# Optimization experiments

Measured on AMD Instinct MI355X. Metric: run time of the kernel, lower is better.

## Reference

```python
import jax, jax.numpy as jnp
import numpy as np

B, T, H = 32, 4096, 512
K = 11  # conv kernel size, 'same' padding


def setup_inputs() -> dict:
    key = jax.random.key(0)
    k1, k2, k3, k4, k5 = jax.random.split(key, 5)
    eh = jax.random.normal(k1, (B, T, H), dtype=jnp.float32)
    dhx = jax.random.normal(k2, (B, H), dtype=jnp.float32)
    ax = jax.random.uniform(k3, (B, T), dtype=jnp.float32)
    conv_w = jax.random.normal(k4, (1, 1, K), dtype=jnp.float32) * 0.1
    conv_b = jax.random.normal(k5, (1,), dtype=jnp.float32) * 0.1
    return {"eh": eh, "dhx": dhx, "ax": ax, "conv_w": conv_w, "conv_b": conv_b}


def reference(eh, dhx, ax, conv_w, conv_b):
    # content score: (B,T,H) . (B,H) -> (B,T)
    pax = jnp.einsum('bth,bh->bt', eh, dhx)
    # location bias: 1D 'same' conv on previous attention vector
    pad = (K - 1) // 2
    loc = jax.lax.conv_general_dilated(
        ax[:, None, :], conv_w,
        window_strides=(1,), padding=[(pad, pad)],
        dimension_numbers=('NCH', 'OIH', 'NCH'))[:, 0, :] + conv_b
    pax = pax + loc
    # softmax over time axis (legacy F.softmax on 2D -> dim=1)
    a = jax.nn.softmax(pax, axis=1)
    # summary: weighted sum over time -> (B,H)
    sx = jnp.einsum('bth,bt->bh', eh, a)
    return (sx, a)
```

## Files before the change

kernel.cpp:

```cpp
#include <hip/hip_runtime.h>
#include <cfloat>

#define BB 32
#define TT 4096
#define HH 512
#define KSZ 11
#define PAD 5
#define TCHUNK 128
#define NCHUNK (TT / TCHUNK)
#define NWAVES 4
#define ROWS_PER_WAVE (TCHUNK / NWAVES)

__global__ __launch_bounds__(256) void attn_pass1(
    const float* __restrict__ eh, const float* __restrict__ dhx,
    const float* __restrict__ ax, const float* __restrict__ conv_w,
    const float* __restrict__ conv_b,
    float* __restrict__ pax_ws, float* __restrict__ part_m,
    float* __restrict__ part_l, float* __restrict__ part_acc)
{
    const int bid  = blockIdx.x;
    const int b    = bid / NCHUNK;
    const int c    = bid % NCHUNK;
    const int tid  = threadIdx.x;
    const int wave = tid >> 6;
    const int lane = tid & 63;

    __shared__ float s_loc[TCHUNK];
    __shared__ float red_m[NWAVES], red_l[NWAVES];
    __shared__ float red_acc[NWAVES][HH];

    if (tid < TCHUNK) {
        const int t = c * TCHUNK + tid;
        float locv = conv_b[0];
        #pragma unroll
        for (int k = 0; k < KSZ; ++k) {
            const int ts = t + k - PAD;
            const float v = (ts >= 0 && ts < TT) ? ax[b * TT + ts] : 0.0f;
            locv = fmaf(v, conv_w[k], locv);
        }
        s_loc[tid] = locv;
    }

    const float4* dp = (const float4*)(dhx + (size_t)b * HH + lane * 8);
    const float4 d0 = dp[0];
    const float4 d1 = dp[1];

    __syncthreads();

    float m = -FLT_MAX, l = 0.0f;
    float acc[8];
    #pragma unroll
    for (int j = 0; j < 8; ++j) acc[j] = 0.0f;

    const int t0 = c * TCHUNK + wave * ROWS_PER_WAVE;
    for (int r = 0; r < ROWS_PER_WAVE; ++r) {
        const int t = t0 + r;
        const float4* ep = (const float4*)(eh + ((size_t)b * TT + t) * HH + lane * 8);
        const float4 e0 = ep[0];
        const float4 e1 = ep[1];

        float dot = e0.x * d0.x + e0.y * d0.y + e0.z * d0.z + e0.w * d0.w
                  + e1.x * d1.x + e1.y * d1.y + e1.z * d1.z + e1.w * d1.w;
        #pragma unroll
        for (int off = 32; off >= 1; off >>= 1)
            dot += __shfl_xor(dot, off, 64);

        const float paxv = dot + s_loc[t - c * TCHUNK];
        if (lane == 0) pax_ws[(size_t)b * TT + t] = paxv;

        const float newm = fmaxf(m, paxv);
        const float sc = __expf(m - newm);
        const float p  = __expf(paxv - newm);
        l = l * sc + p;
        acc[0] = fmaf(p, e0.x, acc[0] * sc);
        acc[1] = fmaf(p, e0.y, acc[1] * sc);
        acc[2] = fmaf(p, e0.z, acc[2] * sc);
        acc[3] = fmaf(p, e0.w, acc[3] * sc);
        acc[4] = fmaf(p, e1.x, acc[4] * sc);
        acc[5] = fmaf(p, e1.y, acc[5] * sc);
        acc[6] = fmaf(p, e1.z, acc[6] * sc);
        acc[7] = fmaf(p, e1.w, acc[7] * sc);
        m = newm;
    }

    float4* ra = (float4*)&red_acc[wave][lane * 8];
    ra[0] = make_float4(acc[0], acc[1], acc[2], acc[3]);
    ra[1] = make_float4(acc[4], acc[5], acc[6], acc[7]);
    if (lane == 0) { red_m[wave] = m; red_l[wave] = l; }
    __syncthreads();

    if (wave == 0) {
        const float M = fmaxf(fmaxf(red_m[0], red_m[1]), fmaxf(red_m[2], red_m[3]));
        float L = 0.0f;
        float o[8];
        #pragma unroll
        for (int j = 0; j < 8; ++j) o[j] = 0.0f;
        #pragma unroll
        for (int w = 0; w < NWAVES; ++w) {
            const float s = __expf(red_m[w] - M);
            L = fmaf(red_l[w], s, L);
            #pragma unroll
            for (int j = 0; j < 8; ++j)
                o[j] = fmaf(red_acc[w][lane * 8 + j], s, o[j]);
        }
        if (lane == 0) { part_m[bid] = M; part_l[bid] = L; }
        float4* pa = (float4*)(part_acc + (size_t)bid * HH + lane * 8);
        pa[0] = make_float4(o[0], o[1], o[2], o[3]);
        pa[1] = make_float4(o[4], o[5], o[6], o[7]);
    }
}

__global__ __launch_bounds__(512) void attn_pass2(
    const float* __restrict__ pax_ws, const float* __restrict__ part_m,
    const float* __restrict__ part_l, const float* __restrict__ part_acc,
    float* __restrict__ out_sx, float* __restrict__ out_a)
{
    const int b = blockIdx.x;
    const int tid = threadIdx.x;

    __shared__ float sm[NCHUNK], sl[NCHUNK];
    if (tid < NCHUNK) {
        sm[tid] = part_m[b * NCHUNK + tid];
        sl[tid] = part_l[b * NCHUNK + tid];
    }
    __syncthreads();

    float M = -FLT_MAX;
    #pragma unroll
    for (int i = 0; i < NCHUNK; ++i) M = fmaxf(M, sm[i]);
    float L = 0.0f;
    #pragma unroll
    for (int i = 0; i < NCHUNK; ++i) L = fmaf(sl[i], __expf(sm[i] - M), L);
    const float invL = 1.0f / L;

    float s = 0.0f;
    #pragma unroll 4
    for (int i = 0; i < NCHUNK; ++i)
        s = fmaf(part_acc[((size_t)b * NCHUNK + i) * HH + tid], __expf(sm[i] - M), s);
    out_sx[b * HH + tid] = s * invL;

    for (int t = tid; t < TT; t += 512)
        out_a[(size_t)b * TT + t] = __expf(pax_ws[(size_t)b * TT + t] - M) * invL;
}

extern "C" void kernel_launch(void* const* d_in, const int* in_sizes, int n_in,
                              void* d_out, int out_size, void* d_ws, size_t ws_size,
                              hipStream_t stream) {
    const float* eh     = (const float*)d_in[0];
    const float* dhx    = (const float*)d_in[1];
    const float* ax     = (const float*)d_in[2];
    const float* conv_w = (const float*)d_in[3];
    const float* conv_b = (const float*)d_in[4];

    float* out    = (float*)d_out;
    float* out_sx = out;
    float* out_a  = out + BB * HH;

    float* pax_ws   = (float*)d_ws;
    float* part_m   = pax_ws + (size_t)BB * TT;
    float* part_l   = part_m + BB * NCHUNK;
    float* part_acc = part_l + BB * NCHUNK;

    attn_pass1<<<BB * NCHUNK, 256, 0, stream>>>(eh, dhx, ax, conv_w, conv_b,
                                                pax_ws, part_m, part_l, part_acc);
    attn_pass2<<<BB, 512, 0, stream>>>(pax_ws, part_m, part_l, part_acc,
                                       out_sx, out_a);
}
```

Baseline: 55.30 us.

## Halve time chunk, branch online-softmax update, split pass2 across more blocks

Pass 1 now uses 64-row time chunks, which doubles the block count, and adds an occupancy hint to launch bounds. The online-softmax update branches on whether the new score exceeds the running max, so the common case skips one exponential and the rescale multiplies. The dot product is rewritten as two FMA chains. Pass 2 runs 8 blocks per batch instead of one, each handling a 64-column slice of the output and a 512-element slice of the attention vector, with chunk weights precomputed in shared memory. The risks are more partial-accumulator traffic from twice as many chunks and possible wave divergence on the new branch.

Measured after the change: 53.85 us. 2.6% less time.

```diff
diff --git a/kernel.cpp b/kernel.cpp
--- a/kernel.cpp
+++ b/kernel.cpp
@@ -6,12 +6,12 @@
 #define HH 512
 #define KSZ 11
 #define PAD 5
-#define TCHUNK 128
+#define TCHUNK 64
 #define NCHUNK (TT / TCHUNK)
 #define NWAVES 4
 #define ROWS_PER_WAVE (TCHUNK / NWAVES)
 
-__global__ __launch_bounds__(256) void attn_pass1(
+__global__ __launch_bounds__(256, 8) void attn_pass1(
     const float* __restrict__ eh, const float* __restrict__ dhx,
     const float* __restrict__ ax, const float* __restrict__ conv_w,
     const float* __restrict__ conv_b,
@@ -59,8 +59,15 @@
         const float4 e0 = ep[0];
         const float4 e1 = ep[1];
 
-        float dot = e0.x * d0.x + e0.y * d0.y + e0.z * d0.z + e0.w * d0.w
-                  + e1.x * d1.x + e1.y * d1.y + e1.z * d1.z + e1.w * d1.w;
+        float da = e0.x * d0.x;
+        da = fmaf(e0.y, d0.y, da);
+        da = fmaf(e0.z, d0.z, da);
+        da = fmaf(e0.w, d0.w, da);
+        float db = e1.x * d1.x;
+        db = fmaf(e1.y, d1.y, db);
+        db = fmaf(e1.z, d1.z, db);
+        db = fmaf(e1.w, d1.w, db);
+        float dot = da + db;
         #pragma unroll
         for (int off = 32; off >= 1; off >>= 1)
             dot += __shfl_xor(dot, off, 64);
@@ -68,19 +75,30 @@
         const float paxv = dot + s_loc[t - c * TCHUNK];
         if (lane == 0) pax_ws[(size_t)b * TT + t] = paxv;
 
-        const float newm = fmaxf(m, paxv);
-        const float sc = __expf(m - newm);
-        const float p  = __expf(paxv - newm);
-        l = l * sc + p;
-        acc[0] = fmaf(p, e0.x, acc[0] * sc);
-        acc[1] = fmaf(p, e0.y, acc[1] * sc);
-        acc[2] = fmaf(p, e0.z, acc[2] * sc);
-        acc[3] = fmaf(p, e0.w, acc[3] * sc);
-        acc[4] = fmaf(p, e1.x, acc[4] * sc);
-        acc[5] = fmaf(p, e1.y, acc[5] * sc);
-        acc[6] = fmaf(p, e1.z, acc[6] * sc);
-        acc[7] = fmaf(p, e1.w, acc[7] * sc);
-        m = newm;
+        if (paxv <= m) {
+            const float p = __expf(paxv - m);
+            l += p;
+            acc[0] = fmaf(p, e0.x, acc[0]);
+            acc[1] = fmaf(p, e0.y, acc[1]);
+            acc[2] = fmaf(p, e0.z, acc[2]);
+            acc[3] = fmaf(p, e0.w, acc[3]);
+            acc[4] = fmaf(p, e1.x, acc[4]);
+            acc[5] = fmaf(p, e1.y, acc[5]);
+            acc[6] = fmaf(p, e1.z, acc[6]);
+            acc[7] = fmaf(p, e1.w, acc[7]);
+        } else {
+            const float sc = __expf(m - paxv);
+            l = fmaf(l, sc, 1.0f);
+            acc[0] = fmaf(acc[0], sc, e0.x);
+            acc[1] = fmaf(acc[1], sc, e0.y);
+            acc[2] = fmaf(acc[2], sc, e0.z);
+            acc[3] = fmaf(acc[3], sc, e0.w);
+            acc[4] = fmaf(acc[4], sc, e1.x);
+            acc[5] = fmaf(acc[5], sc, e1.y);
+            acc[6] = fmaf(acc[6], sc, e1.z);
+            acc[7] = fmaf(acc[7], sc, e1.w);
+            m = paxv;
+        }
     }
 
     float4* ra = (float4*)&red_acc[wave][lane * 8];
@@ -110,37 +128,55 @@
     }
 }
 
-__global__ __launch_bounds__(512) void attn_pass2(
+__global__ __launch_bounds__(256) void attn_pass2(
     const float* __restrict__ pax_ws, const float* __restrict__ part_m,
     const float* __restrict__ part_l, const float* __restrict__ part_acc,
     float* __restrict__ out_sx, float* __restrict__ out_a)
 {
-    const int b = blockIdx.x;
+    const int b   = blockIdx.x >> 3;
+    const int j   = blockIdx.x & 7;
     const int tid = threadIdx.x;
 
-    __shared__ float sm[NCHUNK], sl[NCHUNK];
+    __shared__ float sm_s[NCHUNK], sw[NCHUNK], slw[NCHUNK];
+    __shared__ float sred[4][64];
+
+    if (tid < NCHUNK) sm_s[tid] = part_m[b * NCHUNK + tid];
+    __syncthreads();
+
+    float M = -FLT_MAX;
+    #pragma unroll
+    for (int i = 0; i < NCHUNK; ++i) M = fmaxf(M, sm_s[i]);
+
     if (tid < NCHUNK) {
-        sm[tid] = part_m[b * NCHUNK + tid];
-        sl[tid] = part_l[b * NCHUNK + tid];
-    }
-    __syncthreads();
-
-    float M = -FLT_MAX;
-    #pragma unroll
-    for (int i = 0; i < NCHUNK; ++i) M = fmaxf(M, sm[i]);
+        const float w = __expf(sm_s[tid] - M);
+        sw[tid]  = w;
+        slw[tid] = part_l[b * NCHUNK + tid] * w;
+    }
+    __syncthreads();
+
     float L = 0.0f;
     #pragma unroll
-    for (int i = 0; i < NCHUNK; ++i) L = fmaf(sl[i], __expf(sm[i] - M), L);
+    for (int i = 0; i < NCHUNK; ++i) L += slw[i];
     const float invL = 1.0f / L;
 
-    float s = 0.0f;
-    #pragma unroll 4
-    for (int i = 0; i < NCHUNK; ++i)
-        s = fmaf(part_acc[((size_t)b * NCHUNK + i) * HH + tid], __expf(sm[i] - M), s);
-    out_sx[b * HH + tid] = s * invL;
-
-    for (int t = tid; t < TT; t += 512)
+    const int c  = tid >> 6;
+    const int hh = tid & 63;
+    const int h  = j * 64 + hh;
+    float v = 0.0f;
+    #pragma unroll
+    for (int i = c * 16; i < c * 16 + 16; ++i)
+        v = fmaf(part_acc[((size_t)b * NCHUNK + i) * HH + h], sw[i], v);
+    sred[c][hh] = v;
+    __syncthreads();
+    if (tid < 64)
+        out_sx[b * HH + j * 64 + tid] =
+            (sred[0][tid] + sred[1][tid] + sred[2][tid] + sred[3][tid]) * invL;
+
+    #pragma unroll
+    for (int q = 0; q < 2; ++q) {
+        const int t = j * 512 + q * 256 + tid;
         out_a[(size_t)b * TT + t] = __expf(pax_ws[(size_t)b * TT + t] - M) * invL;
+    }
 }
 
 extern "C" void kernel_launch(void* const* d_in, const int* in_sizes, int n_in,
@@ -163,6 +199,6 @@
 
     attn_pass1<<<BB * NCHUNK, 256, 0, stream>>>(eh, dhx, ax, conv_w, conv_b,
                                                 pax_ws, part_m, part_l, part_acc);
-    attn_pass2<<<BB, 512, 0, stream>>>(pax_ws, part_m, part_l, part_acc,
-                                       out_sx, out_a);
+    attn_pass2<<<BB * 8, 256, 0, stream>>>(pax_ws, part_m, part_l, part_acc,
+                                           out_sx, out_a);
 }
```
